# Kernel tuning notes

Measured on AMD Instinct MI355X. Metric: run time of the kernel, lower is better.

The kernel has to match this reference:

```python
import jax, jax.numpy as jnp
import numpy as np

B, N, H, DH, ORDER, DEG = 64, 256, 8, 64, 4, 16
D = H * DH
TOTAL = B * N
E = TOTAL * DEG


def setup_inputs() -> dict:
    key = jax.random.key(0)
    ks = jax.random.split(key, 16)
    output = jax.random.normal(ks[0], (N, B, D), dtype=jnp.float32)
    # attention weights: positive, row-normalized like softmax output
    attn = jax.nn.softmax(jax.random.normal(ks[1], (B, H, N, N), dtype=jnp.float32), axis=-1)
    out_each_head = jax.random.normal(ks[2], (B, N, H, DH), dtype=jnp.float32)
    # random graph edges, endpoints within the same graph (global node ids)
    g = jax.random.randint(ks[3], (E,), 0, B)
    s = g * N + jax.random.randint(ks[4], (E,), 0, N)
    d = g * N + jax.random.randint(ks[5], (E,), 0, N)
    edge_index = jnp.stack([s, d], axis=0).astype(jnp.int64)
    # full graphs, no padding: feature_indices[:,0]=graph id, [:,1]=node pos
    fi = jnp.stack([jnp.repeat(jnp.arange(B), N), jnp.tile(jnp.arange(N), B)], axis=1).astype(jnp.int64)
    batch = fi[:, 0]
    sc = 0.1
    params = dict(
        W_gcn=jax.random.normal(ks[6], (ORDER, ORDER)) * sc,
        b_gcn=jnp.zeros((ORDER,), jnp.float32),
        W_lin=jax.random.normal(ks[7], (ORDER, ORDER)) * sc,
        b_lin=jnp.zeros((ORDER,), jnp.float32),
        W_cheb=jax.random.normal(ks[8], (ORDER, DH, DH)) * sc,
        b_cheb=jnp.zeros((DH,), jnp.float32),
        W_cat=jax.random.normal(ks[9], (2 * D, D)) * sc,
        b_cat=jnp.zeros((D,), jnp.float32),
        gamma=jnp.ones((D,), jnp.float32),
        beta=jnp.zeros((D,), jnp.float32),
    )
    return dict(output=output, attn=attn, out_each_head=out_each_head,
                edge_index=edge_index, feature_indices=fi, batch=batch, **params)


def reference(output, attn, out_each_head, edge_index, feature_indices, batch,
              W_gcn, b_gcn, W_lin, b_lin, W_cheb, b_cheb, W_cat, b_cat, gamma, beta):
    Bn, Hn, Nn, _ = attn.shape
    C = W_gcn.shape[0]
    total = Bn * Nn
    NT = Hn * total

    # ---- get_filter_coefficients: GCN over fully-connected attention graphs ----
    # edge weights are detached in the original (edge_weight.detach())
    A = jax.lax.stop_gradient(attn).transpose(1, 0, 2, 3).reshape(Hn * Bn, Nn, Nn)
    A_hat = A + jnp.eye(Nn, dtype=A.dtype)  # add self loops (weight 1)
    deg = A_hat.sum(axis=1)                 # deg_j = sum_i A_hat[i,j]
    dinv = jnp.where(deg > 0, jax.lax.rsqrt(deg), 0.0)  # (HB, N)
    # x = ones, so x @ W_gcn is a constant row = column sums of W_gcn
    w_row = W_gcn.sum(axis=0)               # (C,)
    s = jnp.einsum('bi,bij->bj', dinv, A_hat) * dinv     # (HB, N)
    x_c = jnp.tanh(s[:, :, None] * w_row + b_gcn)        # (HB, N, C)
    gap = x_c.mean(axis=1)                  # global avg pool per graph (HB, C)
    coeff = gap @ W_lin + b_lin             # (HB, C) rows ordered (head, batch)

    # ---- dynamic Chebyshev filtering per head on the input graph ----
    offsets = (jnp.arange(Hn) * total).astype(edge_index.dtype)
    src = (edge_index[0][None, :] + offsets[:, None]).reshape(-1)
    dst = (edge_index[1][None, :] + offsets[:, None]).reshape(-1)
    deg_n = jax.ops.segment_sum(jnp.ones(src.shape[0], jnp.float32), dst, num_segments=NT)
    dinv_n = jnp.where(deg_n > 0, jax.lax.rsqrt(deg_n), 0.0)
    norm_e = -(dinv_n[src] * dinv_n[dst])   # scaled Laplacian L_hat = -D^-1/2 A D^-1/2

    def prop(x):  # L_hat @ x via gather/scatter
        return jax.ops.segment_sum(norm_e[:, None] * x[src], dst, num_segments=NT)

    # nodes ordered (head, batch, node)
    x0 = out_each_head.transpose(2, 0, 1, 3).reshape(NT, DH)
    batch_all = (batch[None, :] + (jnp.arange(Hn) * Bn)[:, None]).reshape(-1)  # graph id h*B+b
    c_node = coeff[batch_all]               # (NT, ORDER) per-node dynamic coefficients

    T_prev, T_cur = x0, prop(x0)
    acc = c_node[:, 0:1] * (T_prev @ W_cheb[0]) + c_node[:, 1:2] * (T_cur @ W_cheb[1])
    for k in range(2, C):
        T_next = 2.0 * prop(T_cur) - T_prev
        acc = acc + c_node[:, k:k + 1] * (T_next @ W_cheb[k])
        T_prev, T_cur = T_cur, T_next
    acc = acc + b_cheb                      # (NT, DH)

    # regroup heads: (H, B*N, DH) -> (B*N, H*DH), scatter back to (N, B, D)
    filtered = acc.reshape(Hn, total, DH).transpose(1, 0, 2).reshape(total, Hn * DH)
    out_filtered = jnp.zeros_like(output).at[feature_indices[:, 1], feature_indices[:, 0], :].set(filtered)

    # skip connection + linear_cat + final LayerNorm
    out_cat = jnp.concatenate([output, out_filtered], axis=-1)
    out = out_cat @ W_cat + b_cat
    mu = out.mean(axis=-1, keepdims=True)
    var = ((out - mu) ** 2).mean(axis=-1, keepdims=True)
    out = (out - mu) * jax.lax.rsqrt(var + 1e-5) * gamma + beta
    return out
```

## Files before the change

kernel.cpp:

```cpp
#include <hip/hip_runtime.h>
#include <stdint.h>

#define Bq      64
#define Nq      256
#define Hq      8
#define DHq     64
#define TOTALq  16384
#define NTq     131072
#define Dq      512

typedef __attribute__((ext_vector_type(8))) short short8;
typedef __attribute__((ext_vector_type(4))) float floatx4;

__device__ __forceinline__ unsigned short f2bf(float f) {
    union { float f; unsigned int u; } c; c.f = f;
    unsigned int u = c.u;
    return (unsigned short)((u + 0x7fffu + ((u >> 16) & 1u)) >> 16);
}
__device__ __forceinline__ float bf2f(unsigned short u) {
    union { unsigned int u; float f; } c; c.u = ((unsigned int)u) << 16;
    return c.f;
}


__global__ void count_deg_kernel(const int* __restrict__ dstp, int* __restrict__ cnt, int E) {
    int e = blockIdx.x * 256 + threadIdx.x;
    if (e < E) atomicAdd(&cnt[dstp[e]], 1);
}

__global__ void dinv_kernel(const int* __restrict__ cnt, float* __restrict__ dinv_n) {
    int v = blockIdx.x * 256 + threadIdx.x;
    if (v < TOTALq) {
        int c = cnt[v];
        dinv_n[v] = (c > 0) ? rsqrtf((float)c) : 0.0f;
    }
}

__global__ void pscatter_kernel(const int* __restrict__ srcp, const int* __restrict__ dstp,
                                const float* __restrict__ dinv_n, float* __restrict__ Pf, int E) {
    int e = blockIdx.x * 256 + threadIdx.x;
    if (e >= E) return;
    int s = srcp[e], d = dstp[e];
    int g = d >> 8;
    atomicAdd(&Pf[((size_t)g << 16) + ((size_t)(d & 255) << 8) + (s & 255)],
              -(dinv_n[s] * dinv_n[d]));
}

__global__ void pconv_kernel(const float* __restrict__ Pf, unsigned short* __restrict__ Pb) {
    int i = (blockIdx.x * 256 + threadIdx.x) * 4;
    float4 v = *(const float4*)(Pf + i);
    unsigned int lo = (unsigned int)f2bf(v.x) | ((unsigned int)f2bf(v.y) << 16);
    unsigned int hi = (unsigned int)f2bf(v.z) | ((unsigned int)f2bf(v.w) << 16);
    *(uint2*)(Pb + i) = make_uint2(lo, hi);
}

__global__ void wchebt_kernel(const float* __restrict__ W, float* __restrict__ WT) {
    int idx = blockIdx.x * 256 + threadIdx.x;
    int k = idx >> 12, rem = idx & 4095;
    int n = rem >> 6, j = rem & 63;
    WT[idx] = W[(k << 12) + (j << 6) + n];
}

__global__ __launch_bounds__(512)
void coeff_kernel(const float* __restrict__ attn,
                  const float* __restrict__ Wg, const float* __restrict__ bg,
                  const float* __restrict__ Wlin, const float* __restrict__ blin,
                  float* __restrict__ coeff) {
    __shared__ floatx4 part[8][64];
    __shared__ floatx4 dinv4[64];
    const int g = blockIdx.x;
    const int h = g >> 6;
    const int b = g & 63;
    const float* A = attn + ((size_t)(b * Hq + h)) * (Nq * Nq);
    const int tid = threadIdx.x;
    const int rg = tid >> 6;
    const int cv = tid & 63;
    const float* Ap = A + cv * 4;

    floatx4 s1 = (floatx4){0.f, 0.f, 0.f, 0.f};
#pragma unroll 8
    for (int r = 0; r < 32; ++r)
        s1 += *(const floatx4*)(Ap + (size_t)(rg * 32 + r) * 256);
    part[rg][cv] = s1;
    __syncthreads();

    if (tid < 64) {
        floatx4 cs = part[0][tid];
#pragma unroll
        for (int i = 1; i < 8; ++i) cs += part[i][tid];
        floatx4 dv;
#pragma unroll
        for (int i = 0; i < 4; ++i) dv[i] = rsqrtf(cs[i] + 1.0f);
        dinv4[tid] = dv;
    }
    __syncthreads();

    const float* dsc = (const float*)dinv4;
    floatx4 s2 = (floatx4){0.f, 0.f, 0.f, 0.f};
#pragma unroll 8
    for (int r = 0; r < 32; ++r) {
        int rr = rg * 32 + r;
        s2 += dsc[rr] * (*(const floatx4*)(Ap + (size_t)rr * 256));
    }
    part[rg][cv] = s2;
    __syncthreads();

    if (tid < 64) {
        floatx4 ws = part[0][tid];
#pragma unroll
        for (int i = 1; i < 8; ++i) ws += part[i][tid];
        floatx4 dv = dinv4[tid];
        floatx4 sj = (ws + dv) * dv;

        float wr[4], bgl[4];
#pragma unroll
        for (int c = 0; c < 4; ++c) {
            wr[c]  = Wg[0 * 4 + c] + Wg[1 * 4 + c] + Wg[2 * 4 + c] + Wg[3 * 4 + c];
            bgl[c] = bg[c];
        }
        float v[4];
#pragma unroll
        for (int c = 0; c < 4; ++c) {
            v[c] = tanhf(sj[0] * wr[c] + bgl[c]) + tanhf(sj[1] * wr[c] + bgl[c]) +
                   tanhf(sj[2] * wr[c] + bgl[c]) + tanhf(sj[3] * wr[c] + bgl[c]);
#pragma unroll
            for (int o = 32; o >= 1; o >>= 1) v[c] += __shfl_down(v[c], o, 64);
        }
        float g0 = __shfl(v[0], 0, 64), g1 = __shfl(v[1], 0, 64);
        float g2 = __shfl(v[2], 0, 64), g3 = __shfl(v[3], 0, 64);
        if (tid < 4) {
            float r = blin[tid] + (g0 * Wlin[0 * 4 + tid] + g1 * Wlin[1 * 4 + tid] +
                                   g2 * Wlin[2 * 4 + tid] + g3 * Wlin[3 * 4 + tid]) *
                                      (1.0f / 256.0f);
            coeff[g * 4 + tid] = r;
        }
    }
}

__global__ __launch_bounds__(512, 2)
void cheb_fused(const unsigned short* __restrict__ Pb, const float* __restrict__ oeh,
                const float* __restrict__ WchTf, const float* __restrict__ coeff,
                const float* __restrict__ bch, unsigned short* __restrict__ filtb) {
    extern __shared__ unsigned char sm[];
    unsigned short* cm = (unsigned short*)sm;
    unsigned short* rm = (unsigned short*)(sm + 32768);
    unsigned short* Wl = (unsigned short*)(sm + 65536);

    const int g = blockIdx.x;
    const int b = (g & 7) * 8 + ((g >> 3) & 7);
    const int h = g >> 6;
    const int tid = threadIdx.x;
    const int lane = tid & 63, wv = tid >> 6;
    const int wr = wv >> 1, wc = wv & 1;
    const int quad = lane >> 4, l15 = lane & 15;

    const unsigned short* Pbase = Pb + ((size_t)b << 16);
    const float* cf = coeff + (h * 64 + b) * 4;

    {
        const int sn = tid >> 1;
        const int sh = (tid & 1) * 32;
        const float* sp = oeh + (size_t)(b * 256 + sn) * 512 + h * 64 + sh;
        unsigned int pk[16];
#pragma unroll
        for (int j = 0; j < 8; ++j) {
            float4 v = *(const float4*)(sp + j * 4);
            pk[2 * j]     = (unsigned)f2bf(v.x) | ((unsigned)f2bf(v.y) << 16);
            pk[2 * j + 1] = (unsigned)f2bf(v.z) | ((unsigned)f2bf(v.w) << 16);
        }
#pragma unroll
        for (int jj = 0; jj < 4; ++jj)
            *(uint4*)(rm + sn * 64 + ((((sh >> 3) + jj) ^ (sn & 7)) << 3)) =
                make_uint4(pk[4 * jj], pk[4 * jj + 1], pk[4 * jj + 2], pk[4 * jj + 3]);
#pragma unroll
        for (int e = 0; e < 32; ++e) {
            int c = sh + e;
            unsigned short v =
                (unsigned short)((e & 1) ? (pk[e >> 1] >> 16) : (pk[e >> 1] & 0xffffu));
            cm[c * 256 + (((sn >> 3) ^ (c & 31)) << 3) + (sn & 7)] = v;
        }
        float ck = cf[0];
        int r = tid >> 3, su = tid & 7;
        const float* wp = WchTf + r * 64 + su * 8;
        float4 w0 = *(const float4*)wp, w1 = *(const float4*)(wp + 4);
        *(uint4*)(Wl + r * 72 + su * 8) = make_uint4(
            (unsigned)f2bf(w0.x * ck) | ((unsigned)f2bf(w0.y * ck) << 16),
            (unsigned)f2bf(w0.z * ck) | ((unsigned)f2bf(w0.w * ck) << 16),
            (unsigned)f2bf(w1.x * ck) | ((unsigned)f2bf(w1.y * ck) << 16),
            (unsigned)f2bf(w1.z * ck) | ((unsigned)f2bf(w1.w * ck) << 16));
    }
    __syncthreads();

    unsigned int curp[4][2][2], prvp[4][2][2];
#pragma unroll
    for (int rt = 0; rt < 4; ++rt)
#pragma unroll
        for (int ct = 0; ct < 2; ++ct)
#pragma unroll
            for (int p = 0; p < 2; ++p) {
                int m = wr * 64 + rt * 16 + quad * 4 + 2 * p;
                int c = wc * 32 + ct * 16 + l15;
                curp[rt][ct][p] = *(const unsigned int*)(cm + c * 256 +
                                                         (((m >> 3) ^ (c & 31)) << 3) + (m & 7));
                prvp[rt][ct][p] = 0u;
            }

    floatx4 accf[4][2];
#pragma unroll
    for (int rt = 0; rt < 4; ++rt)
#pragma unroll
        for (int ct = 0; ct < 2; ++ct) accf[rt][ct] = (floatx4){0.f, 0.f, 0.f, 0.f};

#pragma unroll
    for (int k = 0; k < 4; ++k) {
#pragma unroll
        for (int kk = 0; kk < 2; ++kk) {
            short8 af[4], bfw[2];
#pragma unroll
            for (int rt = 0; rt < 4; ++rt) {
                int row = wr * 64 + rt * 16 + l15;
                af[rt] = *(const short8*)(rm + row * 64 + (((kk * 4 + quad) ^ (row & 7)) << 3));
            }
#pragma unroll
            for (int ct = 0; ct < 2; ++ct) {
                int oc = wc * 32 + ct * 16 + l15;
                bfw[ct] = *(const short8*)(Wl + oc * 72 + kk * 32 + quad * 8);
            }
#pragma unroll
            for (int rt = 0; rt < 4; ++rt)
#pragma unroll
                for (int ct = 0; ct < 2; ++ct)
                    accf[rt][ct] = __builtin_amdgcn_mfma_f32_16x16x32_bf16(
                        af[rt], bfw[ct], accf[rt][ct], 0, 0, 0);
        }
        if (k < 3) {
            floatx4 accp[4][2];
#pragma unroll
            for (int rt = 0; rt < 4; ++rt)
#pragma unroll
                for (int ct = 0; ct < 2; ++ct) accp[rt][ct] = (floatx4){0.f, 0.f, 0.f, 0.f};
#pragma unroll
            for (int kt = 0; kt < 8; ++kt) {
                short8 ap[4], bp[2];
#pragma unroll
                for (int rt = 0; rt < 4; ++rt) {
                    int row = wr * 64 + rt * 16 + l15;
                    ap[rt] = *(const short8*)(Pbase + row * 256 + kt * 32 + quad * 8);
                }
#pragma unroll
                for (int ct = 0; ct < 2; ++ct) {
                    int c = wc * 32 + ct * 16 + l15;
                    bp[ct] = *(const short8*)(cm + c * 256 + (((kt * 4 + quad) ^ (c & 31)) << 3));
                }
#pragma unroll
                for (int rt = 0; rt < 4; ++rt)
#pragma unroll
                    for (int ct = 0; ct < 2; ++ct)
                        accp[rt][ct] = __builtin_amdgcn_mfma_f32_16x16x32_bf16(
                            ap[rt], bp[ct], accp[rt][ct], 0, 0, 0);
            }
            __syncthreads();
#pragma unroll
            for (int rt = 0; rt < 4; ++rt)
#pragma unroll
                for (int ct = 0; ct < 2; ++ct)
#pragma unroll
                    for (int p = 0; p < 2; ++p) {
                        float a0 = accp[rt][ct][2 * p], a1 = accp[rt][ct][2 * p + 1];
                        if (k > 0) {
                            unsigned pv = prvp[rt][ct][p];
                            a0 = 2.0f * a0 - bf2f((unsigned short)(pv & 0xffffu));
                            a1 = 2.0f * a1 - bf2f((unsigned short)(pv >> 16));
                        }
                        unsigned nv = (unsigned)f2bf(a0) | ((unsigned)f2bf(a1) << 16);
                        prvp[rt][ct][p] = curp[rt][ct][p];
                        curp[rt][ct][p] = nv;
                        int m = wr * 64 + rt * 16 + quad * 4 + 2 * p;
                        int c = wc * 32 + ct * 16 + l15;
                        if (k < 2)
                            *(unsigned int*)(cm + c * 256 + (((m >> 3) ^ (c & 31)) << 3) +
                                             (m & 7)) = nv;
                        rm[m * 64 + (((c >> 3) ^ (m & 7)) << 3) + (c & 7)] =
                            (unsigned short)(nv & 0xffffu);
                        rm[(m + 1) * 64 + (((c >> 3) ^ ((m + 1) & 7)) << 3) + (c & 7)] =
                            (unsigned short)(nv >> 16);
                    }
            {
                float ck = cf[k + 1];
                int r = tid >> 3, su = tid & 7;
                const float* wp = WchTf + (k + 1) * 4096 + r * 64 + su * 8;
                float4 w0 = *(const float4*)wp, w1 = *(const float4*)(wp + 4);
                *(uint4*)(Wl + r * 72 + su * 8) = make_uint4(
                    (unsigned)f2bf(w0.x * ck) | ((unsigned)f2bf(w0.y * ck) << 16),
                    (unsigned)f2bf(w0.z * ck) | ((unsigned)f2bf(w0.w * ck) << 16),
                    (unsigned)f2bf(w1.x * ck) | ((unsigned)f2bf(w1.y * ck) << 16),
                    (unsigned)f2bf(w1.z * ck) | ((unsigned)f2bf(w1.w * ck) << 16));
            }
            __syncthreads();
        }
    }

    float bias[2];
#pragma unroll
    for (int ct = 0; ct < 2; ++ct) bias[ct] = bch[wc * 32 + ct * 16 + l15];
#pragma unroll
    for (int rt = 0; rt < 4; ++rt)
#pragma unroll
        for (int ct = 0; ct < 2; ++ct) {
            int c = wc * 32 + ct * 16 + l15;
#pragma unroll
            for (int i = 0; i < 4; ++i) {
                int m = wr * 64 + rt * 16 + quad * 4 + i;
                filtb[((size_t)m * 64 + b) * 512 + h * 64 + c] =
                    f2bf(accf[rt][ct][i] + bias[ct]);
            }
        }
}

__global__ void wt2_kernel(const float* __restrict__ W, unsigned short* __restrict__ Wt2) {
    int idx = blockIdx.x * 256 + threadIdx.x;
    int col = idx & 511;
    int ktq = idx >> 9;
    const float* src = W + (size_t)(ktq * 8) * 512 + col;
    unsigned int pk[4];
#pragma unroll
    for (int q2 = 0; q2 < 4; ++q2) {
        unsigned short a = f2bf(src[(q2 * 2 + 0) * 512]);
        unsigned short b = f2bf(src[(q2 * 2 + 1) * 512]);
        pk[q2] = (unsigned int)a | ((unsigned int)b << 16);
    }
    *(uint4*)(Wt2 + (size_t)idx * 8) = make_uint4(pk[0], pk[1], pk[2], pk[3]);
}

__global__ __launch_bounds__(512, 2)
void gemm_ln_mfma(const float* __restrict__ outp, const unsigned short* __restrict__ filtb,
                  const unsigned short* __restrict__ Wt2, const float* __restrict__ bcat,
                  const float* __restrict__ gamma, const float* __restrict__ beta,
                  float* __restrict__ out) {
    extern __shared__ unsigned char smc[];
    unsigned short* A_lds0 = (unsigned short*)smc;
    unsigned short* A_lds1 = (unsigned short*)(smc + 4096);
    float* ep = (float*)smc;

    const int tid = threadIdx.x;
    const int lane = tid & 63;
    const int wv = tid >> 6;
    const int quad = lane >> 4;
    const int l15 = lane & 15;
    const int r0 = blockIdx.x * 64;

    const int s_row = tid >> 3;
    const int s_sub = tid & 7;
    const int s_q   = s_sub >> 1;
    const int s_e   = (s_sub & 1) * 4;

    const size_t boff = (size_t)(quad * 512 + wv * 64 + l15) * 8;

    floatx4 acc[4][4];
#pragma unroll
    for (int rt = 0; rt < 4; ++rt)
#pragma unroll
        for (int ct = 0; ct < 4; ++ct) acc[rt][ct] = (floatx4){0.f, 0.f, 0.f, 0.f};

    short8 bA[4], bB[4];

    {
#pragma unroll
        for (int ct = 0; ct < 4; ++ct)
            bA[ct] = *(const short8*)(Wt2 + boff + ct * 128);
        float4 av = *(const float4*)(outp + (size_t)(r0 + s_row) * 512 + s_sub * 4);
        uint2 ap;
        ap.x = (unsigned int)f2bf(av.x) | ((unsigned int)f2bf(av.y) << 16);
        ap.y = (unsigned int)f2bf(av.z) | ((unsigned int)f2bf(av.w) << 16);
        *(uint2*)(A_lds0 + (s_q * 64 + s_row) * 8 + s_e) = ap;
        __syncthreads();
    }

#define GSTEP(KT, BC, BN, AC, AN, HASNEXT)                                          \
    do {                                                                            \
        const int kt_ = (KT);                                                       \
        const bool hn_ = (HASNEXT);                                                 \
        const bool isf_ = (kt_ + 1 < 16);                                           \
        float4 av_; uint2 afb_;                                                     \
        if (hn_) {                                                                  \
            _Pragma("unroll")                                                       \
            for (int ct = 0; ct < 4; ++ct)                                          \
                BN[ct] = *(const short8*)(Wt2 + (size_t)(kt_ + 1) * 16384 +         \
                                          boff + ct * 128);                         \
            const int kc_ = (kt_ + 1) * 32;                                         \
            if (isf_)                                                               \
                av_ = *(const float4*)(outp + (size_t)(r0 + s_row) * 512 +          \
                                       kc_ + s_sub * 4);                            \
            else                                                                    \
                afb_ = *(const uint2*)(filtb + (size_t)(r0 + s_row) * 512 +         \
                                       (kc_ - 512) + s_sub * 4);                    \
        }                                                                           \
        short8 af_[4];                                                              \
        _Pragma("unroll")                                                           \
        for (int rt = 0; rt < 4; ++rt)                                              \
            af_[rt] = *(const short8*)(AC + (quad * 64 + rt * 16 + l15) * 8);       \
        _Pragma("unroll")                                                           \
        for (int rt = 0; rt < 4; ++rt)                                              \
            _Pragma("unroll")                                                       \
            for (int ct = 0; ct < 4; ++ct)                                          \
                acc[rt][ct] = __builtin_amdgcn_mfma_f32_16x16x32_bf16(              \
                    af_[rt], BC[ct], acc[rt][ct], 0, 0, 0);                         \
        if (hn_) {                                                                  \
            uint2 ap_;                                                              \
            if (isf_) {                                                             \
                ap_.x = (unsigned int)f2bf(av_.x) | ((unsigned int)f2bf(av_.y) << 16); \
                ap_.y = (unsigned int)f2bf(av_.z) | ((unsigned int)f2bf(av_.w) << 16); \
            } else {                                                                \
                ap_ = afb_;                                                         \
            }                                                                       \
            *(uint2*)(AN + (s_q * 64 + s_row) * 8 + s_e) = ap_;                     \
        }                                                                           \
        __syncthreads();                                                            \
    } while (0)

    for (int kt2 = 0; kt2 < 16; ++kt2) {
        GSTEP(2 * kt2,     bA, bB, A_lds0, A_lds1, true);
        GSTEP(2 * kt2 + 1, bB, bA, A_lds1, A_lds0, kt2 < 15);
    }
#undef GSTEP

    float gg[8], bb[8];
#pragma unroll
    for (int i = 0; i < 8; ++i) { gg[i] = gamma[i * 64 + lane]; bb[i] = beta[i * 64 + lane]; }
    float bc[4];
#pragma unroll
    for (int ct = 0; ct < 4; ++ct) bc[ct] = bcat[wv * 64 + ct * 16 + l15];

    for (int half = 0; half < 2; ++half) {
        __syncthreads();
#pragma unroll
        for (int rt2 = 0; rt2 < 2; ++rt2) {
            const int rt = half * 2 + rt2;
#pragma unroll
            for (int ct = 0; ct < 4; ++ct) {
                const int col = wv * 64 + ct * 16 + l15;
#pragma unroll
                for (int i = 0; i < 4; ++i) {
                    const int row_l = rt2 * 16 + quad * 4 + i;
                    ep[row_l * 512 + col] = acc[rt][ct][i] + bc[ct];
                }
            }
        }
        __syncthreads();
#pragma unroll
        for (int m4 = 0; m4 < 4; ++m4) {
            const int m = wv * 4 + m4;
            float s = 0.0f, ss = 0.0f;
#pragma unroll
            for (int i = 0; i < 8; ++i) {
                float v = ep[m * 512 + i * 64 + lane];
                s += v; ss += v * v;
            }
#pragma unroll
            for (int o = 32; o >= 1; o >>= 1) {
                s += __shfl_down(s, o, 64);
                ss += __shfl_down(ss, o, 64);
            }
            s = __shfl(s, 0, 64);
            ss = __shfl(ss, 0, 64);
            const float mu = s * (1.0f / 512.0f);
            const float var = ss * (1.0f / 512.0f) - mu * mu;
            const float rs = rsqrtf(var + 1e-5f);
            const int r = r0 + half * 32 + m;
#pragma unroll
            for (int i = 0; i < 8; ++i) {
                const int d = i * 64 + lane;
                out[(size_t)r * 512 + d] = (ep[m * 512 + d] - mu) * rs * gg[i] + bb[i];
            }
        }
    }
}

extern "C" void kernel_launch(void* const* d_in, const int* in_sizes, int n_in,
                              void* d_out, int out_size, void* d_ws, size_t ws_size,
                              hipStream_t stream) {
    const float* output       = (const float*)d_in[0];
    const float* attn         = (const float*)d_in[1];
    const float* oeh          = (const float*)d_in[2];
    const int*   edge_index   = (const int*)d_in[3];
    const float* W_gcn        = (const float*)d_in[6];
    const float* b_gcn        = (const float*)d_in[7];
    const float* W_lin        = (const float*)d_in[8];
    const float* b_lin        = (const float*)d_in[9];
    const float* W_cheb       = (const float*)d_in[10];
    const float* b_cheb       = (const float*)d_in[11];
    const float* W_cat        = (const float*)d_in[12];
    const float* b_cat        = (const float*)d_in[13];
    const float* gamma        = (const float*)d_in[14];
    const float* beta         = (const float*)d_in[15];
    float* out = (float*)d_out;

    const int E = in_sizes[3] / 2;
    const int* srcp = edge_index;
    const int* dstp = edge_index + E;

    uint8_t* ws = (uint8_t*)d_ws;
    size_t cur = 0;
    auto alloc = [&](size_t bytes) -> void* {
        void* p = ws + cur;
        cur += (bytes + 255) & ~(size_t)255;
        return p;
    };
    int*   cnt     = (int*)alloc(TOTALq * sizeof(int));
    float* dinv_n  = (float*)alloc(TOTALq * sizeof(float));
    float* Pf      = (float*)alloc((size_t)64 * 65536 * sizeof(float));
    unsigned short* Pb   = (unsigned short*)alloc((size_t)64 * 65536 * 2);
    float* coeff   = (float*)alloc(512 * 4 * sizeof(float));
    float* WchTf   = (float*)alloc(4 * 64 * 64 * sizeof(float));
    unsigned short* Wt2  = (unsigned short*)alloc((size_t)Dq * 1024 * 2);
    unsigned short* filtb = (unsigned short*)alloc((size_t)TOTALq * Dq * 2);
    (void)ws_size; (void)n_in; (void)out_size;

    hipMemsetAsync(cnt, 0, TOTALq * sizeof(int), stream);
    count_deg_kernel<<<(E + 255) / 256, 256, 0, stream>>>(dstp, cnt, E);
    dinv_kernel<<<TOTALq / 256, 256, 0, stream>>>(cnt, dinv_n);
    hipMemsetAsync(Pf, 0, (size_t)64 * 65536 * sizeof(float), stream);
    pscatter_kernel<<<(E + 255) / 256, 256, 0, stream>>>(srcp, dstp, dinv_n, Pf, E);
    pconv_kernel<<<4096, 256, 0, stream>>>(Pf, Pb);

    coeff_kernel<<<Hq * Bq, 512, 0, stream>>>(attn, W_gcn, b_gcn, W_lin, b_lin, coeff);
    wt2_kernel<<<256, 256, 0, stream>>>(W_cat, Wt2);
    wchebt_kernel<<<64, 256, 0, stream>>>(W_cheb, WchTf);

    cheb_fused<<<512, 512, 74752, stream>>>(Pb, oeh, WchTf, coeff, b_cheb, filtb);

    gemm_ln_mfma<<<TOTALq / 64, 512, 65536, stream>>>(output, filtb, Wt2, b_cat,
                                                      gamma, beta, out);
}
```

Before: 414.4 us.

## Merge small prep kernels and deepen GEMM prefetch to two stages

Folds the dinv computation into the edge scatter kernel and merges the two weight-transpose kernels into one launch, which removes three small kernel launches. The final GEMM+LayerNorm kernel now prefetches B fragments and A tiles two K-steps ahead instead of one, and swaps __syncthreads for an explicit lgkmcnt wait plus s_barrier, so global loads have more time to land. This uses more registers and relies on the manual waitcnt being enough for correctness.

```diff
diff --git a/kernel.cpp b/kernel.cpp
--- a/kernel.cpp
+++ b/kernel.cpp
@@ -28,22 +28,17 @@
     if (e < E) atomicAdd(&cnt[dstp[e]], 1);
 }
 
-__global__ void dinv_kernel(const int* __restrict__ cnt, float* __restrict__ dinv_n) {
-    int v = blockIdx.x * 256 + threadIdx.x;
-    if (v < TOTALq) {
-        int c = cnt[v];
-        dinv_n[v] = (c > 0) ? rsqrtf((float)c) : 0.0f;
-    }
-}
-
 __global__ void pscatter_kernel(const int* __restrict__ srcp, const int* __restrict__ dstp,
-                                const float* __restrict__ dinv_n, float* __restrict__ Pf, int E) {
+                                const int* __restrict__ cnt, float* __restrict__ Pf, int E) {
     int e = blockIdx.x * 256 + threadIdx.x;
     if (e >= E) return;
     int s = srcp[e], d = dstp[e];
+    int cs = cnt[s], cd = cnt[d];
+    float dvs = (cs > 0) ? rsqrtf((float)cs) : 0.0f;
+    float dvd = (cd > 0) ? rsqrtf((float)cd) : 0.0f;
     int g = d >> 8;
     atomicAdd(&Pf[((size_t)g << 16) + ((size_t)(d & 255) << 8) + (s & 255)],
-              -(dinv_n[s] * dinv_n[d]));
+              -(dvs * dvd));
 }
 
 __global__ void pconv_kernel(const float* __restrict__ Pf, unsigned short* __restrict__ Pb) {
@@ -54,11 +49,28 @@
     *(uint2*)(Pb + i) = make_uint2(lo, hi);
 }
 
-__global__ void wchebt_kernel(const float* __restrict__ W, float* __restrict__ WT) {
-    int idx = blockIdx.x * 256 + threadIdx.x;
-    int k = idx >> 12, rem = idx & 4095;
-    int n = rem >> 6, j = rem & 63;
-    WT[idx] = W[(k << 12) + (j << 6) + n];
+__global__ void prep_kernel(const float* __restrict__ Wcat, unsigned short* __restrict__ Wt2,
+                            const float* __restrict__ Wch, float* __restrict__ WchTf) {
+    int bid = blockIdx.x;
+    if (bid < 256) {
+        int idx = bid * 256 + threadIdx.x;
+        int col = idx & 511;
+        int ktq = idx >> 9;
+        const float* src = Wcat + (size_t)(ktq * 8) * 512 + col;
+        unsigned int pk[4];
+#pragma unroll
+        for (int q2 = 0; q2 < 4; ++q2) {
+            unsigned short a = f2bf(src[(q2 * 2 + 0) * 512]);
+            unsigned short b = f2bf(src[(q2 * 2 + 1) * 512]);
+            pk[q2] = (unsigned int)a | ((unsigned int)b << 16);
+        }
+        *(uint4*)(Wt2 + (size_t)idx * 8) = make_uint4(pk[0], pk[1], pk[2], pk[3]);
+    } else {
+        int idx = (bid - 256) * 256 + threadIdx.x;
+        int k = idx >> 12, rem = idx & 4095;
+        int n = rem >> 6, j = rem & 63;
+        WchTf[idx] = Wch[(k << 12) + (j << 6) + n];
+    }
 }
 
 __global__ __launch_bounds__(512)
@@ -317,21 +329,6 @@
         }
 }
 
-__global__ void wt2_kernel(const float* __restrict__ W, unsigned short* __restrict__ Wt2) {
-    int idx = blockIdx.x * 256 + threadIdx.x;
-    int col = idx & 511;
-    int ktq = idx >> 9;
-    const float* src = W + (size_t)(ktq * 8) * 512 + col;
-    unsigned int pk[4];
-#pragma unroll
-    for (int q2 = 0; q2 < 4; ++q2) {
-        unsigned short a = f2bf(src[(q2 * 2 + 0) * 512]);
-        unsigned short b = f2bf(src[(q2 * 2 + 1) * 512]);
-        pk[q2] = (unsigned int)a | ((unsigned int)b << 16);
-    }
-    *(uint4*)(Wt2 + (size_t)idx * 8) = make_uint4(pk[0], pk[1], pk[2], pk[3]);
-}
-
 __global__ __launch_bounds__(512, 2)
 void gemm_ln_mfma(const float* __restrict__ outp, const unsigned short* __restrict__ filtb,
                   const unsigned short* __restrict__ Wt2, const float* __restrict__ bcat,
@@ -363,12 +360,18 @@
         for (int ct = 0; ct < 4; ++ct) acc[rt][ct] = (floatx4){0.f, 0.f, 0.f, 0.f};
 
     short8 bA[4], bB[4];
+    float4 avX_f, avY_f;
+    uint2  avX_b, avY_b;
 
     {
 #pragma unroll
         for (int ct = 0; ct < 4; ++ct)
             bA[ct] = *(const short8*)(Wt2 + boff + ct * 128);
+#pragma unroll
+        for (int ct = 0; ct < 4; ++ct)
+            bB[ct] = *(const short8*)(Wt2 + (size_t)16384 + boff + ct * 128);
         float4 av = *(const float4*)(outp + (size_t)(r0 + s_row) * 512 + s_sub * 4);
+        avY_f = *(const float4*)(outp + (size_t)(r0 + s_row) * 512 + 32 + s_sub * 4);
         uint2 ap;
         ap.x = (unsigned int)f2bf(av.x) | ((unsigned int)f2bf(av.y) << 16);
         ap.y = (unsigned int)f2bf(av.z) | ((unsigned int)f2bf(av.w) << 16);
@@ -376,24 +379,17 @@
         __syncthreads();
     }
 
-#define GSTEP(KT, BC, BN, AC, AN, HASNEXT)                                          \
+#define GSTEP(KT, BCUR, AC, AN, AVCF, AVCB, AVNF, AVNB)                             \
     do {                                                                            \
         const int kt_ = (KT);                                                       \
-        const bool hn_ = (HASNEXT);                                                 \
-        const bool isf_ = (kt_ + 1 < 16);                                           \
-        float4 av_; uint2 afb_;                                                     \
-        if (hn_) {                                                                  \
-            _Pragma("unroll")                                                       \
-            for (int ct = 0; ct < 4; ++ct)                                          \
-                BN[ct] = *(const short8*)(Wt2 + (size_t)(kt_ + 1) * 16384 +         \
-                                          boff + ct * 128);                         \
-            const int kc_ = (kt_ + 1) * 32;                                         \
-            if (isf_)                                                               \
-                av_ = *(const float4*)(outp + (size_t)(r0 + s_row) * 512 +          \
-                                       kc_ + s_sub * 4);                            \
+        if (kt_ <= 29) {                                                            \
+            const int kc2_ = (kt_ + 2) * 32;                                        \
+            if (kc2_ < 512)                                                         \
+                AVNF = *(const float4*)(outp + (size_t)(r0 + s_row) * 512 +         \
+                                        kc2_ + s_sub * 4);                          \
             else                                                                    \
-                afb_ = *(const uint2*)(filtb + (size_t)(r0 + s_row) * 512 +         \
-                                       (kc_ - 512) + s_sub * 4);                    \
+                AVNB = *(const uint2*)(filtb + (size_t)(r0 + s_row) * 512 +         \
+                                       (kc2_ - 512) + s_sub * 4);                   \
         }                                                                           \
         short8 af_[4];                                                              \
         _Pragma("unroll")                                                           \
@@ -404,23 +400,31 @@
             _Pragma("unroll")                                                       \
             for (int ct = 0; ct < 4; ++ct)                                          \
                 acc[rt][ct] = __builtin_amdgcn_mfma_f32_16x16x32_bf16(              \
-                    af_[rt], BC[ct], acc[rt][ct], 0, 0, 0);                         \
-        if (hn_) {                                                                  \
+                    af_[rt], BCUR[ct], acc[rt][ct], 0, 0, 0);                       \
+        if (kt_ <= 29) {                                                            \
+            _Pragma("unroll")                                                       \
+            for (int ct = 0; ct < 4; ++ct)                                          \
+                BCUR[ct] = *(const short8*)(Wt2 + (size_t)(kt_ + 2) * 16384 +       \
+                                            boff + ct * 128);                       \
+        }                                                                           \
+        if (kt_ <= 30) {                                                            \
             uint2 ap_;                                                              \
-            if (isf_) {                                                             \
-                ap_.x = (unsigned int)f2bf(av_.x) | ((unsigned int)f2bf(av_.y) << 16); \
-                ap_.y = (unsigned int)f2bf(av_.z) | ((unsigned int)f2bf(av_.w) << 16); \
+            if ((kt_ + 1) * 32 < 512) {                                             \
+                ap_.x = (unsigned int)f2bf(AVCF.x) | ((unsigned int)f2bf(AVCF.y) << 16); \
+                ap_.y = (unsigned int)f2bf(AVCF.z) | ((unsigned int)f2bf(AVCF.w) << 16); \
             } else {                                                                \
-                ap_ = afb_;                                                         \
+                ap_ = AVCB;                                                         \
             }                                                                       \
             *(uint2*)(AN + (s_q * 64 + s_row) * 8 + s_e) = ap_;                     \
         }                                                                           \
-        __syncthreads();                                                            \
+        asm volatile("s_waitcnt lgkmcnt(0)" ::: "memory");                          \
+        __builtin_amdgcn_s_barrier();                                               \
+        __builtin_amdgcn_sched_barrier(0);                                          \
     } while (0)
 
     for (int kt2 = 0; kt2 < 16; ++kt2) {
-        GSTEP(2 * kt2,     bA, bB, A_lds0, A_lds1, true);
-        GSTEP(2 * kt2 + 1, bB, bA, A_lds1, A_lds0, kt2 < 15);
+        GSTEP(2 * kt2,     bA, A_lds0, A_lds1, avY_f, avY_b, avX_f, avX_b);
+        GSTEP(2 * kt2 + 1, bB, A_lds1, A_lds0, avX_f, avX_b, avY_f, avY_b);
     }
 #undef GSTEP
 
@@ -507,7 +511,6 @@
         return p;
     };
     int*   cnt     = (int*)alloc(TOTALq * sizeof(int));
-    float* dinv_n  = (float*)alloc(TOTALq * sizeof(float));
     float* Pf      = (float*)alloc((size_t)64 * 65536 * sizeof(float));
     unsigned short* Pb   = (unsigned short*)alloc((size_t)64 * 65536 * 2);
     float* coeff   = (float*)alloc(512 * 4 * sizeof(float));
@@ -518,14 +521,12 @@
 
     hipMemsetAsync(cnt, 0, TOTALq * sizeof(int), stream);
     count_deg_kernel<<<(E + 255) / 256, 256, 0, stream>>>(dstp, cnt, E);
-    dinv_kernel<<<TOTALq / 256, 256, 0, stream>>>(cnt, dinv_n);
     hipMemsetAsync(Pf, 0, (size_t)64 * 65536 * sizeof(float), stream);
-    pscatter_kernel<<<(E + 255) / 256, 256, 0, stream>>>(srcp, dstp, dinv_n, Pf, E);
+    pscatter_kernel<<<(E + 255) / 256, 256, 0, stream>>>(srcp, dstp, cnt, Pf, E);
     pconv_kernel<<<4096, 256, 0, stream>>>(Pf, Pb);
 
     coeff_kernel<<<Hq * Bq, 512, 0, stream>>>(attn, W_gcn, b_gcn, W_lin, b_lin, coeff);
-    wt2_kernel<<<256, 256, 0, stream>>>(W_cat, Wt2);
-    wchebt_kernel<<<64, 256, 0, stream>>>(W_cheb, WchTf);
+    prep_kernel<<<320, 256, 0, stream>>>(W_cat, Wt2, W_cheb, WchTf);
 
     cheb_fused<<<512, 512, 74752, stream>>>(Pb, oeh, WchTf, coeff, b_cheb, filtb);
 
```

Result: faster. 402.9 us (-2.8%).
